# Optimization experiments

Hardware: AMD Instinct MI355X
Metric: run time of the kernel (lower is better)

The kernel has to match this reference:

```python
import jax, jax.numpy as jnp
import numpy as np

N_NODES = 100000
N_EDGES = 1600000
D_IN = 256
D_OUT = 256


def setup_inputs() -> dict:
    key = jax.random.key(0)
    k1, k2, k3, k4, k5 = jax.random.split(key, 5)
    feat = jax.random.normal(k1, (N_NODES, D_IN), dtype=jnp.float32)
    src = jax.random.randint(k2, (N_EDGES,), 0, N_NODES, dtype=jnp.int32)
    dst = jax.random.randint(k3, (N_EDGES,), 0, N_NODES, dtype=jnp.int32)
    # xavier_uniform with gain for relu (sqrt(2)), as in reset_parameters
    gain = float(np.sqrt(2.0))
    limit = gain * float(np.sqrt(6.0 / (D_IN + D_OUT)))
    w_neigh = jax.random.uniform(k4, (D_OUT, D_IN), minval=-limit, maxval=limit, dtype=jnp.float32)
    w_self = jax.random.uniform(k5, (D_OUT, D_IN), minval=-limit, maxval=limit, dtype=jnp.float32)
    b_self = jnp.zeros((D_OUT,), dtype=jnp.float32)
    return {"feat": feat, "src": src, "dst": dst,
            "w_neigh": w_neigh, "w_self": w_self, "b_self": b_self}


def reference(feat, src, dst, w_neigh, w_self, b_self):
    # SAGEConv, aggregator_type='mean', feat_drop=0, no edge_weight.
    # lin_before_mp = (in_feats > out_feats) = False -> aggregate raw feats first.
    n = feat.shape[0]
    # gather messages at edges and segment-sum into dst nodes
    summed = jax.ops.segment_sum(feat[src], dst, num_segments=n)  # [N, D_in]
    deg = jax.ops.segment_sum(jnp.ones_like(dst, dtype=feat.dtype), dst, num_segments=n)
    h_neigh_raw = summed / jnp.maximum(deg, 1.0)[:, None]  # mean; 0 for isolated nodes
    h_neigh = h_neigh_raw @ w_neigh.T                       # fc_neigh (no bias)
    rst = feat @ w_self.T + b_self + h_neigh                # fc_self(h_self) + h_neigh
    return rst
```

## Files before the change

### kernel.cpp

```cpp
#include <hip/hip_runtime.h>
#include <cstddef>

#define N_NODES 100000
#define N_EDGES 1600000
#define D 256

typedef short          s16x8 __attribute__((ext_vector_type(8)));
typedef unsigned short u16x8 __attribute__((ext_vector_type(8)));
typedef float          f32x4 __attribute__((ext_vector_type(4)));
typedef float          f32x8 __attribute__((ext_vector_type(8)));

__device__ __forceinline__ unsigned short f2bf(float f) {
    unsigned int u = __float_as_uint(f);
    unsigned int r = (u + 0x7fffu + ((u >> 16) & 1u)) >> 16;
    return (unsigned short)r;
}
__device__ __forceinline__ float bf2f(unsigned short u) {
    return __uint_as_float(((unsigned int)u) << 16);
}

#define WS_COUNTS 0
#define WS_ROWPTR (N_NODES)
#define WS_COL    (2 * N_NODES + 16)
#define WS_PART   (WS_COL + N_EDGES)
#define WB_BYTE   ((size_t)(WS_PART + 128) * 4)
#define FB_BYTE   (WB_BYTE + 2 * 65536 * 2)
#define FB_SZ     ((size_t)N_NODES * D * 2)
#define HB2_BYTE  (FB_BYTE + FB_SZ)
#define NEED_LARGE (FB_BYTE + FB_SZ)
#define NEED_XL    (HB2_BYTE + FB_SZ)
#define NEED_MID   (FB_BYTE)

#define EBLOCKS ((N_EDGES + 255) / 256)
#define FBLOCKS (N_NODES * D / 8 / 256)
#define SCAN_NB ((N_NODES + 1023) / 1024)

__global__ __launch_bounds__(256) void cvt_hist_kernel(
    const float* __restrict__ feat, const float* __restrict__ w_self,
    const float* __restrict__ w_neigh, const int* __restrict__ dst,
    unsigned short* __restrict__ fb, unsigned short* __restrict__ wb,
    int* __restrict__ counts)
{
    const int b = blockIdx.x;
    if (b < FBLOCKS) {
        const int i = b * 256 + threadIdx.x;
        const f32x8 v = ((const f32x8*)feat)[i];
        ushort4 a, c;
        a.x = f2bf(v[0]); a.y = f2bf(v[1]); a.z = f2bf(v[2]); a.w = f2bf(v[3]);
        c.x = f2bf(v[4]); c.y = f2bf(v[5]); c.z = f2bf(v[6]); c.w = f2bf(v[7]);
        ((ushort4*)fb)[i * 2 + 0] = a;
        ((ushort4*)fb)[i * 2 + 1] = c;
    } else if (b < FBLOCKS + 128) {
        const int i = (b - FBLOCKS) * 256 + threadIdx.x;
        const bool isself = (i < 16384);
        const float* srcp = isself ? w_self : w_neigh;
        const int j = (isself ? i : i - 16384) * 4;
        const float4 v = *(const float4*)(srcp + j);
        ushort4 o;
        o.x = f2bf(v.x); o.y = f2bf(v.y); o.z = f2bf(v.z); o.w = f2bf(v.w);
        ((ushort4*)wb)[i] = o;
    } else {
        const int i = (b - FBLOCKS - 128) * 256 + threadIdx.x;
        if (i < N_EDGES) atomicAdd(&counts[dst[i]], 1);
    }
}

__global__ __launch_bounds__(256) void wcvt_hist_kernel(
    const float* __restrict__ w_self, const float* __restrict__ w_neigh,
    const int* __restrict__ dst, unsigned short* __restrict__ wb,
    int* __restrict__ counts)
{
    const int b = blockIdx.x;
    if (b < 128) {
        const int i = b * 256 + threadIdx.x;
        const bool isself = (i < 16384);
        const float* srcp = isself ? w_self : w_neigh;
        const int j = (isself ? i : i - 16384) * 4;
        const float4 v = *(const float4*)(srcp + j);
        ushort4 o;
        o.x = f2bf(v.x); o.y = f2bf(v.y); o.z = f2bf(v.z); o.w = f2bf(v.w);
        ((ushort4*)wb)[i] = o;
    } else {
        const int i = (b - 128) * 256 + threadIdx.x;
        if (i < N_EDGES) atomicAdd(&counts[dst[i]], 1);
    }
}

__global__ __launch_bounds__(1024) void scan_block_kernel(
    const int* __restrict__ counts, int* __restrict__ row_ptr,
    int* __restrict__ partials)
{
    __shared__ int wsum[16];
    const int t = threadIdx.x, b = blockIdx.x, i = b * 1024 + t;
    const int lane = t & 63, w = t >> 6;
    int x = (i < N_NODES) ? counts[i] : 0;
#pragma unroll
    for (int off = 1; off < 64; off <<= 1) {
        int y = __shfl_up(x, off, 64);
        if (lane >= off) x += y;
    }
    if (lane == 63) wsum[w] = x;
    __syncthreads();
    if (w == 0) {
        int s = (lane < 16) ? wsum[lane] : 0;
#pragma unroll
        for (int off = 1; off < 16; off <<= 1) {
            int y = __shfl_up(s, off, 64);
            if (lane >= off) s += y;
        }
        if (lane < 16) wsum[lane] = s;
    }
    __syncthreads();
    const int incl = x + (w > 0 ? wsum[w - 1] : 0);
    if (i < N_NODES) row_ptr[i + 1] = incl;
    if (t == 1023) partials[b] = incl;
}

__global__ __launch_bounds__(1024) void scan_add2_kernel(
    const int* __restrict__ partials, int* __restrict__ row_ptr)
{
    __shared__ int sp[SCAN_NB];
    const int t = threadIdx.x, b = blockIdx.x;
    if (t < SCAN_NB) sp[t] = partials[t];
    __syncthreads();
    int off = 0;
    for (int j = 0; j < b; ++j) off += sp[j];
    const int i = b * 1024 + t;
    if (i < N_NODES) row_ptr[i + 1] += off;
    if (b == 0 && t == 0) row_ptr[0] = 0;
}

__global__ __launch_bounds__(256) void fill_kernel(
    const int* __restrict__ src, const int* __restrict__ dst,
    const int* __restrict__ row_ptr, int* __restrict__ counts,
    int* __restrict__ col)
{
    const int i = blockIdx.x * 256 + threadIdx.x;
    if (i < N_EDGES) {
        const int d = dst[i];
        const int pos = atomicSub(&counts[d], 1) - 1;
        col[row_ptr[d] + pos] = src[i];
    }
}

template <bool OUTBF16>
__global__ __launch_bounds__(256) void aggregate2_kernel(
    const unsigned short* __restrict__ featb,
    const int* __restrict__ row_ptr, const int* __restrict__ col,
    float* __restrict__ outf, unsigned short* __restrict__ outb)
{
    const int node = (blockIdx.x * blockDim.x + threadIdx.x) >> 6;
    const int lane = threadIdx.x & 63;
    if (node >= N_NODES) return;
    const int beg = row_ptr[node], end = row_ptr[node + 1];
    const int half = lane >> 5;
    const int chunk = lane & 31;

    float a0[8] = {0,0,0,0,0,0,0,0};
    float a1[8] = {0,0,0,0,0,0,0,0};
    float a2[8] = {0,0,0,0,0,0,0,0};
    float a3[8] = {0,0,0,0,0,0,0,0};

    const unsigned short* fbp = featb + chunk * 8;

    int j = beg + half;
    for (; j + 6 < end; j += 8) {
        const int s0 = col[j], s1 = col[j + 2], s2 = col[j + 4], s3 = col[j + 6];
        const u16x8 u0 = *(const u16x8*)(fbp + (size_t)s0 * D);
        const u16x8 u1 = *(const u16x8*)(fbp + (size_t)s1 * D);
        const u16x8 u2 = *(const u16x8*)(fbp + (size_t)s2 * D);
        const u16x8 u3 = *(const u16x8*)(fbp + (size_t)s3 * D);
#pragma unroll
        for (int i = 0; i < 8; ++i) a0[i] += bf2f(u0[i]);
#pragma unroll
        for (int i = 0; i < 8; ++i) a1[i] += bf2f(u1[i]);
#pragma unroll
        for (int i = 0; i < 8; ++i) a2[i] += bf2f(u2[i]);
#pragma unroll
        for (int i = 0; i < 8; ++i) a3[i] += bf2f(u3[i]);
    }
    for (; j < end; j += 2) {
        const int s0 = col[j];
        const u16x8 u0 = *(const u16x8*)(fbp + (size_t)s0 * D);
#pragma unroll
        for (int i = 0; i < 8; ++i) a0[i] += bf2f(u0[i]);
    }

    const float invd = 1.0f / fmaxf((float)(end - beg), 1.0f);
    float t[8];
#pragma unroll
    for (int i = 0; i < 8; ++i) {
        float v = (a0[i] + a1[i]) + (a2[i] + a3[i]);
        v += __shfl_xor(v, 32, 64);
        t[i] = v * invd;
    }

    if (OUTBF16) {
        if (half == 0) {
            u16x8 o;
#pragma unroll
            for (int i = 0; i < 8; ++i) o[i] = f2bf(t[i]);
            *(u16x8*)(outb + (size_t)node * D + chunk * 8) = o;
        }
    } else {
        float4 o;
        o.x = t[half * 4 + 0]; o.y = t[half * 4 + 1];
        o.z = t[half * 4 + 2]; o.w = t[half * 4 + 3];
        *(float4*)(outf + (size_t)node * D + chunk * 8 + half * 4) = o;
    }
}

#define GBM 128
#define GBK 64

__global__ __launch_bounds__(256) void gemm_v3_kernel(
    const unsigned short* __restrict__ fb,
    const unsigned short* __restrict__ hb,
    const unsigned short* __restrict__ wb,
    const float* __restrict__ b_self,
    float* __restrict__ outp)
{
    __shared__ unsigned short As[GBM * GBK];

    const int t    = threadIdx.x;
    const int lane = t & 63;
    const int w    = t >> 6;
    const int wr   = w >> 1, wc = w & 1;
    const int row0 = (blockIdx.x >> 1) * GBM;
    const int c0   = (blockIdx.x & 1) * 128 + wc * 64;
    const int nl   = lane & 15;
    const int kg   = lane >> 4;

    const int tr = t >> 1;
    const int th = t & 1;
    int grow = row0 + tr; if (grow > N_NODES - 1) grow = N_NODES - 1;
    const size_t gbrow = (size_t)grow * D;

    int wsw[4];
#pragma unroll
    for (int c = 0; c < 4; ++c) {
        const int cs = th * 32 + c * 8;
        wsw[c] = tr * GBK + (cs ^ ((tr & 7) << 3));
    }
    int rsw[4][2];
#pragma unroll
    for (int m = 0; m < 4; ++m) {
        const int r = wr * 64 + m * 16 + nl;
#pragma unroll
        for (int kk = 0; kk < 2; ++kk) {
            const int cs = kg * 8 + kk * 32;
            rsw[m][kk] = r * GBK + (cs ^ ((r & 7) << 3));
        }
    }

    f32x4 acc[4][4];
#pragma unroll
    for (int m = 0; m < 4; ++m)
#pragma unroll
        for (int n = 0; n < 4; ++n) acc[m][n] = (f32x4){0.f, 0.f, 0.f, 0.f};

    u16x8 st[4];
#pragma unroll
    for (int c = 0; c < 4; ++c)
        st[c] = *(const u16x8*)(fb + gbrow + th * 32 + c * 8);

#pragma unroll
    for (int s = 0; s < 8; ++s) {
#pragma unroll
        for (int c = 0; c < 4; ++c) *(u16x8*)&As[wsw[c]] = st[c];
        __syncthreads();

        if (s < 7) {
            const unsigned short* ap = (s + 1 < 4) ? fb : hb;
            const int koff = ((s + 1) & 3) * 64 + th * 32;
#pragma unroll
            for (int c = 0; c < 4; ++c)
                st[c] = *(const u16x8*)(ap + gbrow + koff + c * 8);
        }

        const int hsel = (s < 4) ? 0 : 65536;
        const int kbase = (s & 3) * 64;
#pragma unroll
        for (int kk = 0; kk < 2; ++kk) {
            s16x8 a[4], b[4];
#pragma unroll
            for (int m = 0; m < 4; ++m)
                a[m] = *(const s16x8*)&As[rsw[m][kk]];
#pragma unroll
            for (int n = 0; n < 4; ++n)
                b[n] = *(const s16x8*)(wb + hsel
                        + (size_t)(c0 + n * 16 + nl) * 256 + kbase + kk * 32 + kg * 8);
#pragma unroll
            for (int m = 0; m < 4; ++m)
#pragma unroll
                for (int n = 0; n < 4; ++n)
                    acc[m][n] = __builtin_amdgcn_mfma_f32_16x16x32_bf16(
                        a[m], b[n], acc[m][n], 0, 0, 0);
        }
        __syncthreads();
    }

#pragma unroll
    for (int n = 0; n < 4; ++n) {
        const float bias = b_self[c0 + n * 16 + nl];
#pragma unroll
        for (int m = 0; m < 4; ++m) {
            const int rbase = row0 + wr * 64 + m * 16 + kg * 4;
#pragma unroll
            for (int r = 0; r < 4; ++r) {
                const int row = rbase + r;
                if (row < N_NODES)
                    outp[(size_t)row * D + c0 + n * 16 + nl] = acc[m][n][r] + bias;
            }
        }
    }
}

__global__ __launch_bounds__(256) void aggregate_f32_kernel(
    const float* __restrict__ feat, const int* __restrict__ row_ptr,
    const int* __restrict__ col, float* __restrict__ outf)
{
    const int node = (blockIdx.x * blockDim.x + threadIdx.x) >> 6;
    const int lane = threadIdx.x & 63;
    if (node >= N_NODES) return;
    const int beg = row_ptr[node], end = row_ptr[node + 1];

    float4 a0 = make_float4(0.f, 0.f, 0.f, 0.f);
    float4 a1 = make_float4(0.f, 0.f, 0.f, 0.f);
    float4 a2 = make_float4(0.f, 0.f, 0.f, 0.f);
    float4 a3 = make_float4(0.f, 0.f, 0.f, 0.f);

#define ACC(acc, s)                                                          \
    do {                                                                     \
        const float4 v = ((const float4*)(feat + (size_t)(s) * D))[lane];    \
        acc.x += v.x; acc.y += v.y; acc.z += v.z; acc.w += v.w;              \
    } while (0)

    int j = beg;
    for (; j + 3 < end; j += 4) {
        const int s0 = col[j], s1 = col[j + 1], s2 = col[j + 2], s3 = col[j + 3];
        ACC(a0, s0); ACC(a1, s1); ACC(a2, s2); ACC(a3, s3);
    }
    for (; j < end; ++j) { const int s0 = col[j]; ACC(a0, s0); }
#undef ACC

    const float invd = 1.0f / fmaxf((float)(end - beg), 1.0f);
    float4 r;
    r.x = ((a0.x + a1.x) + (a2.x + a3.x)) * invd;
    r.y = ((a0.y + a1.y) + (a2.y + a3.y)) * invd;
    r.z = ((a0.z + a1.z) + (a2.z + a3.z)) * invd;
    r.w = ((a0.w + a1.w) + (a2.w + a3.w)) * invd;
    ((float4*)(outf + (size_t)node * D))[lane] = r;
}

__global__ __launch_bounds__(256) void gemm_mfma64_f32h_kernel(
    const float* __restrict__ feat,
    const unsigned short* __restrict__ wb,
    const float* __restrict__ b_self,
    const float* h32,
    float* outp)
{
    const int lane = threadIdx.x & 63;
    const int wslice = threadIdx.x >> 6;
    const int row0 = blockIdx.x * 64;
    const int c0 = wslice * 64;
    const int nl = lane & 15;
    const int kg = lane >> 4;

    f32x4 acc[4][4];
#pragma unroll
    for (int m = 0; m < 4; ++m)
#pragma unroll
        for (int n = 0; n < 4; ++n) acc[m][n] = (f32x4){0.f, 0.f, 0.f, 0.f};

    size_t aoff[4];
#pragma unroll
    for (int m = 0; m < 4; ++m) {
        int r = row0 + m * 16 + nl;
        if (r > N_NODES - 1) r = N_NODES - 1;
        aoff[m] = (size_t)r * D + kg * 8;
    }

#pragma unroll
    for (int hf = 0; hf < 2; ++hf) {
        const unsigned short* wh = wb + hf * 65536 + (size_t)(c0 + nl) * 256 + kg * 8;
#pragma unroll
        for (int kk = 0; kk < 8; ++kk) {
            const int kb = kk * 32;
            s16x8 afrag[4];
#pragma unroll
            for (int m = 0; m < 4; ++m) {
                const float* ap = hf == 0 ? (const float*)feat : h32;
                const f32x8 av = *(const f32x8*)(ap + aoff[m] + kb);
#pragma unroll
                for (int i = 0; i < 8; ++i) afrag[m][i] = (short)f2bf(av[i]);
            }
            s16x8 bfrag[4];
#pragma unroll
            for (int n = 0; n < 4; ++n)
                bfrag[n] = *(const s16x8*)(wh + n * 4096 + kb);
#pragma unroll
            for (int m = 0; m < 4; ++m)
#pragma unroll
                for (int n = 0; n < 4; ++n)
                    acc[m][n] = __builtin_amdgcn_mfma_f32_16x16x32_bf16(
                        afrag[m], bfrag[n], acc[m][n], 0, 0, 0);
        }
    }

    __syncthreads();

#pragma unroll
    for (int n = 0; n < 4; ++n) {
        const float bias = b_self[c0 + n * 16 + nl];
#pragma unroll
        for (int m = 0; m < 4; ++m) {
            const int rbase = row0 + m * 16 + kg * 4;
#pragma unroll
            for (int r = 0; r < 4; ++r) {
                const int row = rbase + r;
                if (row < N_NODES)
                    outp[(size_t)row * D + c0 + n * 16 + nl] = acc[m][n][r] + bias;
            }
        }
    }
}

__global__ __launch_bounds__(256) void scatter_kernel(
    const float* __restrict__ feat, const int* __restrict__ src,
    const int* __restrict__ dst, float* __restrict__ S, float* __restrict__ deg)
{
    const int gtid = blockIdx.x * blockDim.x + threadIdx.x;
    const int wave = gtid >> 6;
    const int lane = gtid & 63;
    const int nwaves = (gridDim.x * blockDim.x) >> 6;
    for (int e = wave; e < N_EDGES; e += nwaves) {
        const int s = src[e];
        const int d = dst[e];
        if (lane == 0) unsafeAtomicAdd(&deg[d], 1.0f);
        const float4 v = ((const float4*)(feat + (size_t)s * D))[lane];
        float* o = S + (size_t)d * D + lane * 4;
        unsafeAtomicAdd(o + 0, v.x);
        unsafeAtomicAdd(o + 1, v.y);
        unsafeAtomicAdd(o + 2, v.z);
        unsafeAtomicAdd(o + 3, v.w);
    }
}

#define BM 64
#define BK 16

__global__ __launch_bounds__(256) void fused_gemm_f32(
    const float* __restrict__ feat, const float* __restrict__ w_neigh,
    const float* __restrict__ w_self, const float* __restrict__ b_self,
    const float* __restrict__ deg, float* out)
{
    __shared__ float At[BK][BM + 4];
    __shared__ float Bt[BK][256];

    const int tid = threadIdx.x;
    const int i0 = blockIdx.x * BM;
    const int trow = tid >> 4;
    const int tcol = tid & 15;
    const int m_load = tid >> 2;
    const int kq = tid & 3;

    const int arow = i0 + m_load;
    const bool arow_ok = arow < N_NODES;
    float invd = 1.0f;
    if (arow_ok) invd = 1.0f / fmaxf(deg[arow], 1.0f);

    float acc[4][16];
#pragma unroll
    for (int r = 0; r < 4; ++r)
#pragma unroll
        for (int c = 0; c < 16; ++c) acc[r][c] = 0.0f;

    for (int kc = 0; kc < (2 * D) / BK; ++kc) {
        const int kb = kc * BK;
        const bool self_part = (kb < D);
        const int kbase = self_part ? kb : (kb - D);

        float4 va = make_float4(0.f, 0.f, 0.f, 0.f);
        if (arow_ok) {
            const float* ap = self_part ? feat : out;
            va = *(const float4*)(ap + (size_t)arow * D + kbase + kq * 4);
            if (!self_part) { va.x *= invd; va.y *= invd; va.z *= invd; va.w *= invd; }
        }
        const float* W = self_part ? w_self : w_neigh;
        const float4* wp = (const float4*)(W + (size_t)tid * D + kbase);
        const float4 w0 = wp[0], w1 = wp[1], w2 = wp[2], w3 = wp[3];

        __syncthreads();
        At[kq * 4 + 0][m_load] = va.x;
        At[kq * 4 + 1][m_load] = va.y;
        At[kq * 4 + 2][m_load] = va.z;
        At[kq * 4 + 3][m_load] = va.w;
        Bt[ 0][tid] = w0.x; Bt[ 1][tid] = w0.y; Bt[ 2][tid] = w0.z; Bt[ 3][tid] = w0.w;
        Bt[ 4][tid] = w1.x; Bt[ 5][tid] = w1.y; Bt[ 6][tid] = w1.z; Bt[ 7][tid] = w1.w;
        Bt[ 8][tid] = w2.x; Bt[ 9][tid] = w2.y; Bt[10][tid] = w2.z; Bt[11][tid] = w2.w;
        Bt[12][tid] = w3.x; Bt[13][tid] = w3.y; Bt[14][tid] = w3.z; Bt[15][tid] = w3.w;
        __syncthreads();

#pragma unroll
        for (int k = 0; k < BK; ++k) {
            const float4 a = *(const float4*)&At[k][trow * 4];
            float4 b[4];
#pragma unroll
            for (int g = 0; g < 4; ++g)
                b[g] = *(const float4*)&Bt[k][g * 64 + tcol * 4];
            const float av[4] = {a.x, a.y, a.z, a.w};
#pragma unroll
            for (int r = 0; r < 4; ++r)
#pragma unroll
                for (int g = 0; g < 4; ++g) {
                    acc[r][g * 4 + 0] = fmaf(av[r], b[g].x, acc[r][g * 4 + 0]);
                    acc[r][g * 4 + 1] = fmaf(av[r], b[g].y, acc[r][g * 4 + 1]);
                    acc[r][g * 4 + 2] = fmaf(av[r], b[g].z, acc[r][g * 4 + 2]);
                    acc[r][g * 4 + 3] = fmaf(av[r], b[g].w, acc[r][g * 4 + 3]);
                }
        }
    }

    float4 bias[4];
#pragma unroll
    for (int g = 0; g < 4; ++g)
        bias[g] = *(const float4*)&b_self[g * 64 + tcol * 4];

#pragma unroll
    for (int r = 0; r < 4; ++r) {
        const int row = i0 + trow * 4 + r;
        if (row < N_NODES) {
            float* op = out + (size_t)row * D;
#pragma unroll
            for (int g = 0; g < 4; ++g) {
                float4 v;
                v.x = acc[r][g * 4 + 0] + bias[g].x;
                v.y = acc[r][g * 4 + 1] + bias[g].y;
                v.z = acc[r][g * 4 + 2] + bias[g].z;
                v.w = acc[r][g * 4 + 3] + bias[g].w;
                *(float4*)(op + g * 64 + tcol * 4) = v;
            }
        }
    }
}

extern "C" void kernel_launch(void* const* d_in, const int* in_sizes, int n_in,
                              void* d_out, int out_size, void* d_ws, size_t ws_size,
                              hipStream_t stream) {
    const float* feat    = (const float*)d_in[0];
    const int*   src     = (const int*)d_in[1];
    const int*   dst     = (const int*)d_in[2];
    const float* w_neigh = (const float*)d_in[3];
    const float* w_self  = (const float*)d_in[4];
    const float* b_self  = (const float*)d_in[5];
    float* out = (float*)d_out;

    const int ablocks  = (N_NODES * 64 + 255) / 256;
    const int g64blks  = (N_NODES + 63) / 64;
    const int gv3blks  = ((N_NODES + GBM - 1) / GBM) * 2;

    if (ws_size >= NEED_MID) {
        int* wsI     = (int*)d_ws;
        int* counts  = wsI + WS_COUNTS;
        int* row_ptr = wsI + WS_ROWPTR;
        int* col     = wsI + WS_COL;
        int* part    = wsI + WS_PART;
        unsigned short* wb = (unsigned short*)((char*)d_ws + WB_BYTE);
        unsigned short* fb = (unsigned short*)((char*)d_ws + FB_BYTE);
        unsigned short* hb = (unsigned short*)((char*)d_ws + HB2_BYTE);

        hipMemsetAsync(counts, 0, N_NODES * sizeof(int), stream);
        if (ws_size >= NEED_LARGE)
            cvt_hist_kernel<<<FBLOCKS + 128 + EBLOCKS, 256, 0, stream>>>(
                feat, w_self, w_neigh, dst, fb, wb, counts);
        else
            wcvt_hist_kernel<<<128 + EBLOCKS, 256, 0, stream>>>(
                w_self, w_neigh, dst, wb, counts);
        scan_block_kernel<<<SCAN_NB, 1024, 0, stream>>>(counts, row_ptr, part);
        scan_add2_kernel<<<SCAN_NB, 1024, 0, stream>>>(part, row_ptr);
        fill_kernel<<<EBLOCKS, 256, 0, stream>>>(src, dst, row_ptr, counts, col);

        if (ws_size >= NEED_XL) {
            aggregate2_kernel<true><<<ablocks, 256, 0, stream>>>(
                fb, row_ptr, col, nullptr, hb);
            gemm_v3_kernel<<<gv3blks, 256, 0, stream>>>(fb, hb, wb, b_self, out);
        } else if (ws_size >= NEED_LARGE) {
            aggregate2_kernel<false><<<ablocks, 256, 0, stream>>>(
                fb, row_ptr, col, out, nullptr);
            gemm_mfma64_f32h_kernel<<<g64blks, 256, 0, stream>>>(
                feat, wb, b_self, out, out);
        } else {
            aggregate_f32_kernel<<<ablocks, 256, 0, stream>>>(
                feat, row_ptr, col, out);
            gemm_mfma64_f32h_kernel<<<g64blks, 256, 0, stream>>>(
                feat, wb, b_self, out, out);
        }
    } else {
        float* deg = (float*)d_ws;
        hipMemsetAsync(out, 0, (size_t)N_NODES * D * sizeof(float), stream);
        hipMemsetAsync(deg, 0, (size_t)N_NODES * sizeof(float), stream);
        scatter_kernel<<<4096, 256, 0, stream>>>(feat, src, dst, out, deg);
        fused_gemm_f32<<<(N_NODES + BM - 1) / BM, 256, 0, stream>>>(
            feat, w_neigh, w_self, b_self, deg, out);
    }
}
```

Measured before the change: 422.2 us.

## Overlap self-GEMM with neighbor aggregation in a mixed-role kernel

Replaces the aggregate-then-fused-GEMM pair with a mega kernel whose blocks interleave roles: every 17th block computes the self-projection GEMM tile (feat@W_self + bias) while the rest do the gather-mean aggregation into a bf16 buffer. A separate neighbor GEMM then adds h_neigh@W_neigh into the output with a read-modify-write. The aim is to hide the compute-bound self GEMM behind the memory-bound gather, at the cost of an extra read and write of the fp32 output and smaller GEMM tiles.

```diff
diff --git a/kernel.cpp b/kernel.cpp
--- a/kernel.cpp
+++ b/kernel.cpp
@@ -26,16 +26,19 @@
 #define WB_BYTE   ((size_t)(WS_PART + 128) * 4)
 #define FB_BYTE   (WB_BYTE + 2 * 65536 * 2)
 #define FB_SZ     ((size_t)N_NODES * D * 2)
-#define HB2_BYTE  (FB_BYTE + FB_SZ)
+#define HB_BYTE   (FB_BYTE + FB_SZ)
+#define NEED_XL   (HB_BYTE + FB_SZ)
 #define NEED_LARGE (FB_BYTE + FB_SZ)
-#define NEED_XL    (HB2_BYTE + FB_SZ)
-#define NEED_MID   (FB_BYTE)
+#define NEED_MID  (FB_BYTE)
 
 #define EBLOCKS ((N_EDGES + 255) / 256)
 #define FBLOCKS (N_NODES * D / 8 / 256)
 #define SCAN_NB ((N_NODES + 1023) / 1024)
-
-__global__ __launch_bounds__(256) void cvt_hist_kernel(
+#define GEMMBLKS ((N_NODES + 63) / 64)
+#define MEGA_R 17
+#define MEGA_NB (GEMMBLKS * MEGA_R)
+
+__global__ __launch_bounds__(256) void cvt_hist_bf16_kernel(
     const float* __restrict__ feat, const float* __restrict__ w_self,
     const float* __restrict__ w_neigh, const int* __restrict__ dst,
     unsigned short* __restrict__ fb, unsigned short* __restrict__ wb,
@@ -143,11 +146,252 @@
     }
 }
 
-template <bool OUTBF16>
-__global__ __launch_bounds__(256) void aggregate2_kernel(
+__global__ __launch_bounds__(256) void mega_kernel(
+    const unsigned short* __restrict__ fb,
+    const unsigned short* __restrict__ wb,
+    const float* __restrict__ b_self,
+    const int* __restrict__ row_ptr, const int* __restrict__ col,
+    unsigned short* __restrict__ hb,
+    float* __restrict__ outp)
+{
+    __shared__ unsigned short As[64 * 64];
+
+    const int bid = blockIdx.x;
+    if (bid % MEGA_R == MEGA_R - 1) {
+        const int gidx = bid / MEGA_R;
+        const int lane = threadIdx.x & 63;
+        const int w    = threadIdx.x >> 6;
+        const int row0 = gidx * 64;
+        const int c0   = w * 64;
+        const int nl   = lane & 15;
+        const int kg   = lane >> 4;
+        const int tr   = threadIdx.x >> 2;
+        const int tq   = threadIdx.x & 3;
+        int grow = row0 + tr; if (grow > N_NODES - 1) grow = N_NODES - 1;
+        const size_t gf = (size_t)grow * D;
+
+        int wsw[2];
+#pragma unroll
+        for (int c = 0; c < 2; ++c) {
+            const int cs = tq * 16 + c * 8;
+            wsw[c] = tr * 64 + (cs ^ ((tr & 7) << 3));
+        }
+        int rsw[4][2];
+#pragma unroll
+        for (int m = 0; m < 4; ++m) {
+            const int r = m * 16 + nl;
+#pragma unroll
+            for (int kk = 0; kk < 2; ++kk) {
+                const int cs = kg * 8 + kk * 32;
+                rsw[m][kk] = r * 64 + (cs ^ ((r & 7) << 3));
+            }
+        }
+
+        f32x4 acc[4][4];
+#pragma unroll
+        for (int m = 0; m < 4; ++m)
+#pragma unroll
+            for (int n = 0; n < 4; ++n) acc[m][n] = (f32x4){0.f, 0.f, 0.f, 0.f};
+
+        u16x8 st0 = *(const u16x8*)(fb + gf + tq * 16);
+        u16x8 st1 = *(const u16x8*)(fb + gf + tq * 16 + 8);
+
+#pragma unroll
+        for (int s = 0; s < 4; ++s) {
+            *(u16x8*)&As[wsw[0]] = st0;
+            *(u16x8*)&As[wsw[1]] = st1;
+            __syncthreads();
+            if (s < 3) {
+                const int koff = (s + 1) * 64 + tq * 16;
+                st0 = *(const u16x8*)(fb + gf + koff);
+                st1 = *(const u16x8*)(fb + gf + koff + 8);
+            }
+            const int kbase = s * 64;
+#pragma unroll
+            for (int kk = 0; kk < 2; ++kk) {
+                s16x8 a[4], b[4];
+#pragma unroll
+                for (int m = 0; m < 4; ++m)
+                    a[m] = *(const s16x8*)&As[rsw[m][kk]];
+#pragma unroll
+                for (int n = 0; n < 4; ++n)
+                    b[n] = *(const s16x8*)(wb
+                            + (size_t)(c0 + n * 16 + nl) * 256 + kbase + kk * 32 + kg * 8);
+#pragma unroll
+                for (int m = 0; m < 4; ++m)
+#pragma unroll
+                    for (int n = 0; n < 4; ++n)
+                        acc[m][n] = __builtin_amdgcn_mfma_f32_16x16x32_bf16(
+                            a[m], b[n], acc[m][n], 0, 0, 0);
+            }
+            __syncthreads();
+        }
+
+#pragma unroll
+        for (int n = 0; n < 4; ++n) {
+            const float bias = b_self[c0 + n * 16 + nl];
+#pragma unroll
+            for (int m = 0; m < 4; ++m) {
+                const int rbase = row0 + m * 16 + kg * 4;
+#pragma unroll
+                for (int r = 0; r < 4; ++r) {
+                    const int row = rbase + r;
+                    if (row < N_NODES)
+                        outp[(size_t)row * D + c0 + n * 16 + nl] = acc[m][n][r] + bias;
+                }
+            }
+        }
+    } else {
+        const int aidx = bid - bid / MEGA_R;
+        const int node = aidx * 4 + (threadIdx.x >> 6);
+        const int lane = threadIdx.x & 63;
+        if (node >= N_NODES) return;
+        const int beg = row_ptr[node], end = row_ptr[node + 1];
+        const int half = lane >> 5;
+        const int chunk = lane & 31;
+
+        float a0[8] = {0,0,0,0,0,0,0,0};
+        float a1[8] = {0,0,0,0,0,0,0,0};
+        float a2[8] = {0,0,0,0,0,0,0,0};
+        float a3[8] = {0,0,0,0,0,0,0,0};
+        const unsigned short* fbp = fb + chunk * 8;
+
+        int j = beg + half;
+        for (; j + 6 < end; j += 8) {
+            const int s0 = col[j], s1 = col[j + 2], s2 = col[j + 4], s3 = col[j + 6];
+            const u16x8 u0 = *(const u16x8*)(fbp + (size_t)s0 * D);
+            const u16x8 u1 = *(const u16x8*)(fbp + (size_t)s1 * D);
+            const u16x8 u2 = *(const u16x8*)(fbp + (size_t)s2 * D);
+            const u16x8 u3 = *(const u16x8*)(fbp + (size_t)s3 * D);
+#pragma unroll
+            for (int i = 0; i < 8; ++i) a0[i] += bf2f(u0[i]);
+#pragma unroll
+            for (int i = 0; i < 8; ++i) a1[i] += bf2f(u1[i]);
+#pragma unroll
+            for (int i = 0; i < 8; ++i) a2[i] += bf2f(u2[i]);
+#pragma unroll
+            for (int i = 0; i < 8; ++i) a3[i] += bf2f(u3[i]);
+        }
+        for (; j < end; j += 2) {
+            const int s0 = col[j];
+            const u16x8 u0 = *(const u16x8*)(fbp + (size_t)s0 * D);
+#pragma unroll
+            for (int i = 0; i < 8; ++i) a0[i] += bf2f(u0[i]);
+        }
+
+        const float invd = 1.0f / fmaxf((float)(end - beg), 1.0f);
+        float tv[8];
+#pragma unroll
+        for (int i = 0; i < 8; ++i) {
+            float v = (a0[i] + a1[i]) + (a2[i] + a3[i]);
+            v += __shfl_xor(v, 32, 64);
+            tv[i] = v * invd;
+        }
+        if (half == 0) {
+            u16x8 o;
+#pragma unroll
+            for (int i = 0; i < 8; ++i) o[i] = f2bf(tv[i]);
+            *(u16x8*)(hb + (size_t)node * D + chunk * 8) = o;
+        }
+    }
+}
+
+__global__ __launch_bounds__(256) void gemm_neigh_kernel(
+    const unsigned short* __restrict__ hb,
+    const unsigned short* __restrict__ wb,
+    float* __restrict__ outp)
+{
+    __shared__ unsigned short As[64 * 64];
+
+    const int lane = threadIdx.x & 63;
+    const int w    = threadIdx.x >> 6;
+    const int row0 = blockIdx.x * 64;
+    const int c0   = w * 64;
+    const int nl   = lane & 15;
+    const int kg   = lane >> 4;
+    const int tr   = threadIdx.x >> 2;
+    const int tq   = threadIdx.x & 3;
+    int grow = row0 + tr; if (grow > N_NODES - 1) grow = N_NODES - 1;
+    const size_t gf = (size_t)grow * D;
+
+    int wsw[2];
+#pragma unroll
+    for (int c = 0; c < 2; ++c) {
+        const int cs = tq * 16 + c * 8;
+        wsw[c] = tr * 64 + (cs ^ ((tr & 7) << 3));
+    }
+    int rsw[4][2];
+#pragma unroll
+    for (int m = 0; m < 4; ++m) {
+        const int r = m * 16 + nl;
+#pragma unroll
+        for (int kk = 0; kk < 2; ++kk) {
+            const int cs = kg * 8 + kk * 32;
+            rsw[m][kk] = r * 64 + (cs ^ ((r & 7) << 3));
+        }
+    }
+
+    f32x4 acc[4][4];
+#pragma unroll
+    for (int m = 0; m < 4; ++m)
+#pragma unroll
+        for (int n = 0; n < 4; ++n) acc[m][n] = (f32x4){0.f, 0.f, 0.f, 0.f};
+
+    u16x8 st0 = *(const u16x8*)(hb + gf + tq * 16);
+    u16x8 st1 = *(const u16x8*)(hb + gf + tq * 16 + 8);
+
+#pragma unroll
+    for (int s = 0; s < 4; ++s) {
+        *(u16x8*)&As[wsw[0]] = st0;
+        *(u16x8*)&As[wsw[1]] = st1;
+        __syncthreads();
+        if (s < 3) {
+            const int koff = (s + 1) * 64 + tq * 16;
+            st0 = *(const u16x8*)(hb + gf + koff);
+            st1 = *(const u16x8*)(hb + gf + koff + 8);
+        }
+        const int kbase = s * 64;
+#pragma unroll
+        for (int kk = 0; kk < 2; ++kk) {
+            s16x8 a[4], b[4];
+#pragma unroll
+            for (int m = 0; m < 4; ++m)
+                a[m] = *(const s16x8*)&As[rsw[m][kk]];
+#pragma unroll
+            for (int n = 0; n < 4; ++n)
+                b[n] = *(const s16x8*)(wb + 65536
+                        + (size_t)(c0 + n * 16 + nl) * 256 + kbase + kk * 32 + kg * 8);
+#pragma unroll
+            for (int m = 0; m < 4; ++m)
+#pragma unroll
+                for (int n = 0; n < 4; ++n)
+                    acc[m][n] = __builtin_amdgcn_mfma_f32_16x16x32_bf16(
+                        a[m], b[n], acc[m][n], 0, 0, 0);
+        }
+        __syncthreads();
+    }
+
+#pragma unroll
+    for (int n = 0; n < 4; ++n) {
+#pragma unroll
+        for (int m = 0; m < 4; ++m) {
+            const int rbase = row0 + m * 16 + kg * 4;
+#pragma unroll
+            for (int r = 0; r < 4; ++r) {
+                const int row = rbase + r;
+                if (row < N_NODES) {
+                    float* p = outp + (size_t)row * D + c0 + n * 16 + nl;
+                    *p = *p + acc[m][n][r];
+                }
+            }
+        }
+    }
+}
+
+__global__ __launch_bounds__(256) void aggregate2f_kernel(
     const unsigned short* __restrict__ featb,
     const int* __restrict__ row_ptr, const int* __restrict__ col,
-    float* __restrict__ outf, unsigned short* __restrict__ outb)
+    float* __restrict__ outf)
 {
     const int node = (blockIdx.x * blockDim.x + threadIdx.x) >> 6;
     const int lane = threadIdx.x & 63;
@@ -160,7 +404,6 @@
     float a1[8] = {0,0,0,0,0,0,0,0};
     float a2[8] = {0,0,0,0,0,0,0,0};
     float a3[8] = {0,0,0,0,0,0,0,0};
-
     const unsigned short* fbp = featb + chunk * 8;
 
     int j = beg + half;
@@ -187,133 +430,17 @@
     }
 
     const float invd = 1.0f / fmaxf((float)(end - beg), 1.0f);
-    float t[8];
+    float tv[8];
 #pragma unroll
     for (int i = 0; i < 8; ++i) {
         float v = (a0[i] + a1[i]) + (a2[i] + a3[i]);
         v += __shfl_xor(v, 32, 64);
-        t[i] = v * invd;
-    }
-
-    if (OUTBF16) {
-        if (half == 0) {
-            u16x8 o;
-#pragma unroll
-            for (int i = 0; i < 8; ++i) o[i] = f2bf(t[i]);
-            *(u16x8*)(outb + (size_t)node * D + chunk * 8) = o;
-        }
-    } else {
-        float4 o;
-        o.x = t[half * 4 + 0]; o.y = t[half * 4 + 1];
-        o.z = t[half * 4 + 2]; o.w = t[half * 4 + 3];
-        *(float4*)(outf + (size_t)node * D + chunk * 8 + half * 4) = o;
-    }
-}
-
-#define GBM 128
-#define GBK 64
-
-__global__ __launch_bounds__(256) void gemm_v3_kernel(
-    const unsigned short* __restrict__ fb,
-    const unsigned short* __restrict__ hb,
-    const unsigned short* __restrict__ wb,
-    const float* __restrict__ b_self,
-    float* __restrict__ outp)
-{
-    __shared__ unsigned short As[GBM * GBK];
-
-    const int t    = threadIdx.x;
-    const int lane = t & 63;
-    const int w    = t >> 6;
-    const int wr   = w >> 1, wc = w & 1;
-    const int row0 = (blockIdx.x >> 1) * GBM;
-    const int c0   = (blockIdx.x & 1) * 128 + wc * 64;
-    const int nl   = lane & 15;
-    const int kg   = lane >> 4;
-
-    const int tr = t >> 1;
-    const int th = t & 1;
-    int grow = row0 + tr; if (grow > N_NODES - 1) grow = N_NODES - 1;
-    const size_t gbrow = (size_t)grow * D;
-
-    int wsw[4];
-#pragma unroll
-    for (int c = 0; c < 4; ++c) {
-        const int cs = th * 32 + c * 8;
-        wsw[c] = tr * GBK + (cs ^ ((tr & 7) << 3));
-    }
-    int rsw[4][2];
-#pragma unroll
-    for (int m = 0; m < 4; ++m) {
-        const int r = wr * 64 + m * 16 + nl;
-#pragma unroll
-        for (int kk = 0; kk < 2; ++kk) {
-            const int cs = kg * 8 + kk * 32;
-            rsw[m][kk] = r * GBK + (cs ^ ((r & 7) << 3));
-        }
-    }
-
-    f32x4 acc[4][4];
-#pragma unroll
-    for (int m = 0; m < 4; ++m)
-#pragma unroll
-        for (int n = 0; n < 4; ++n) acc[m][n] = (f32x4){0.f, 0.f, 0.f, 0.f};
-
-    u16x8 st[4];
-#pragma unroll
-    for (int c = 0; c < 4; ++c)
-        st[c] = *(const u16x8*)(fb + gbrow + th * 32 + c * 8);
-
-#pragma unroll
-    for (int s = 0; s < 8; ++s) {
-#pragma unroll
-        for (int c = 0; c < 4; ++c) *(u16x8*)&As[wsw[c]] = st[c];
-        __syncthreads();
-
-        if (s < 7) {
-            const unsigned short* ap = (s + 1 < 4) ? fb : hb;
-            const int koff = ((s + 1) & 3) * 64 + th * 32;
-#pragma unroll
-            for (int c = 0; c < 4; ++c)
-                st[c] = *(const u16x8*)(ap + gbrow + koff + c * 8);
-        }
-
-        const int hsel = (s < 4) ? 0 : 65536;
-        const int kbase = (s & 3) * 64;
-#pragma unroll
-        for (int kk = 0; kk < 2; ++kk) {
-            s16x8 a[4], b[4];
-#pragma unroll
-            for (int m = 0; m < 4; ++m)
-                a[m] = *(const s16x8*)&As[rsw[m][kk]];
-#pragma unroll
-            for (int n = 0; n < 4; ++n)
-                b[n] = *(const s16x8*)(wb + hsel
-                        + (size_t)(c0 + n * 16 + nl) * 256 + kbase + kk * 32 + kg * 8);
-#pragma unroll
-            for (int m = 0; m < 4; ++m)
-#pragma unroll
-                for (int n = 0; n < 4; ++n)
-                    acc[m][n] = __builtin_amdgcn_mfma_f32_16x16x32_bf16(
-                        a[m], b[n], acc[m][n], 0, 0, 0);
-        }
-        __syncthreads();
-    }
-
-#pragma unroll
-    for (int n = 0; n < 4; ++n) {
-        const float bias = b_self[c0 + n * 16 + nl];
-#pragma unroll
-        for (int m = 0; m < 4; ++m) {
-            const int rbase = row0 + wr * 64 + m * 16 + kg * 4;
-#pragma unroll
-            for (int r = 0; r < 4; ++r) {
-                const int row = rbase + r;
-                if (row < N_NODES)
-                    outp[(size_t)row * D + c0 + n * 16 + nl] = acc[m][n][r] + bias;
-            }
-        }
-    }
+        tv[i] = v * invd;
+    }
+    float4 o;
+    o.x = tv[half * 4 + 0]; o.y = tv[half * 4 + 1];
+    o.z = tv[half * 4 + 2]; o.w = tv[half * 4 + 3];
+    *(float4*)(outf + (size_t)node * D + chunk * 8 + half * 4) = o;
 }
 
 __global__ __launch_bounds__(256) void aggregate_f32_kernel(
@@ -357,8 +484,7 @@
     const float* __restrict__ feat,
     const unsigned short* __restrict__ wb,
     const float* __restrict__ b_self,
-    const float* h32,
-    float* outp)
+    const float* h32, float* outp)
 {
     const int lane = threadIdx.x & 63;
     const int wslice = threadIdx.x >> 6;
@@ -556,9 +682,7 @@
     const float* b_self  = (const float*)d_in[5];
     float* out = (float*)d_out;
 
-    const int ablocks  = (N_NODES * 64 + 255) / 256;
-    const int g64blks  = (N_NODES + 63) / 64;
-    const int gv3blks  = ((N_NODES + GBM - 1) / GBM) * 2;
+    const int ablocks = (N_NODES * 64 + 255) / 256;
 
     if (ws_size >= NEED_MID) {
         int* wsI     = (int*)d_ws;
@@ -568,11 +692,11 @@
         int* part    = wsI + WS_PART;
         unsigned short* wb = (unsigned short*)((char*)d_ws + WB_BYTE);
         unsigned short* fb = (unsigned short*)((char*)d_ws + FB_BYTE);
-        unsigned short* hb = (unsigned short*)((char*)d_ws + HB2_BYTE);
+        unsigned short* hb = (unsigned short*)((char*)d_ws + HB_BYTE);
 
         hipMemsetAsync(counts, 0, N_NODES * sizeof(int), stream);
         if (ws_size >= NEED_LARGE)
-            cvt_hist_kernel<<<FBLOCKS + 128 + EBLOCKS, 256, 0, stream>>>(
+            cvt_hist_bf16_kernel<<<FBLOCKS + 128 + EBLOCKS, 256, 0, stream>>>(
                 feat, w_self, w_neigh, dst, fb, wb, counts);
         else
             wcvt_hist_kernel<<<128 + EBLOCKS, 256, 0, stream>>>(
@@ -582,18 +706,18 @@
         fill_kernel<<<EBLOCKS, 256, 0, stream>>>(src, dst, row_ptr, counts, col);
 
         if (ws_size >= NEED_XL) {
-            aggregate2_kernel<true><<<ablocks, 256, 0, stream>>>(
-                fb, row_ptr, col, nullptr, hb);
-            gemm_v3_kernel<<<gv3blks, 256, 0, stream>>>(fb, hb, wb, b_self, out);
+            mega_kernel<<<MEGA_NB, 256, 0, stream>>>(
+                fb, wb, b_self, row_ptr, col, hb, out);
+            gemm_neigh_kernel<<<GEMMBLKS, 256, 0, stream>>>(hb, wb, out);
         } else if (ws_size >= NEED_LARGE) {
-            aggregate2_kernel<false><<<ablocks, 256, 0, stream>>>(
-                fb, row_ptr, col, out, nullptr);
-            gemm_mfma64_f32h_kernel<<<g64blks, 256, 0, stream>>>(
+            aggregate2f_kernel<<<ablocks, 256, 0, stream>>>(
+                fb, row_ptr, col, out);
+            gemm_mfma64_f32h_kernel<<<GEMMBLKS, 256, 0, stream>>>(
                 feat, wb, b_self, out, out);
         } else {
             aggregate_f32_kernel<<<ablocks, 256, 0, stream>>>(
                 feat, row_ptr, col, out);
-            gemm_mfma64_f32h_kernel<<<g64blks, 256, 0, stream>>>(
+            gemm_mfma64_f32h_kernel<<<GEMMBLKS, 256, 0, stream>>>(
                 feat, wb, b_self, out, out);
         }
     } else {
```

Measured after the change: 491.0 us. 16.3% more time.
